# Kernel optimization log

Measured on AMD Instinct MI355X. Metric: run time of the kernel, lower is better.

The kernel has to match this reference:

```python
import jax, jax.numpy as jnp
import numpy as np


def setup_inputs() -> dict:
    B, I, H = 4096, 512, 1024
    key = jax.random.key(0)
    ks = jax.random.split(key, 10)
    return {
        "input": jax.random.normal(ks[0], (B, I), dtype=jnp.float32),
        "t": jax.random.uniform(ks[1], (B, 1), dtype=jnp.float32),
        "hx": jax.random.normal(ks[2], (B, H), dtype=jnp.float32),
        "cx": jax.random.normal(ks[3], (B, H), dtype=jnp.float32),
        "weight_ih": jax.random.normal(ks[4], (4 * H, I), dtype=jnp.float32),
        "weight_hh": jax.random.normal(ks[5], (4 * H, H), dtype=jnp.float32),
        "bias_ih": jax.random.normal(ks[6], (4 * H,), dtype=jnp.float32),
        "bias_hh": jax.random.normal(ks[7], (4 * H,), dtype=jnp.float32),
        "W_decomp": jax.random.normal(ks[8], (H, H), dtype=jnp.float32),
        "b_decomp": jax.random.normal(ks[9], (H,), dtype=jnp.float32),
    }


def reference(input, t, hx, cx, weight_ih, weight_hh, bias_ih, bias_hh, W_decomp, b_decomp):
    H = W_decomp.shape[0]
    # gates: [B, 4H]
    gates = input @ weight_ih.T + bias_ih + hx @ weight_hh.T + bias_hh
    ingate, forgetgate, cellgate, outgate = jnp.split(gates, 4, axis=1)
    # time-decay factor g(t): elementwise 1/t where t != 0, broadcast [B,1] -> [B,H]
    T = jnp.where(t != 0, 1.0 / jnp.where(t != 0, t, 1.0), 0.0)  # [B, 1]
    T = jnp.broadcast_to(T, (t.shape[0], H))
    # T-LSTM cell-state decomposition
    C_ST = jnp.tanh(cx @ W_decomp + b_decomp)
    cx_adj = cx - C_ST + T * C_ST
    ingate = jax.nn.sigmoid(ingate)
    forgetgate = jax.nn.sigmoid(forgetgate)
    cellgate = jnp.tanh(cellgate)
    outgate = jax.nn.sigmoid(outgate)
    cy = forgetgate * cx_adj + ingate * cellgate
    hy = outgate * jnp.tanh(cy)
    return (hy, cy)
```

## Files before the change

### kernel.cpp

```cpp
#include <hip/hip_runtime.h>
#include <cstdint>


typedef __attribute__((ext_vector_type(8))) __bf16 bf16x8;
typedef __attribute__((ext_vector_type(4))) float f32x4;

__device__ __forceinline__ unsigned short f2bf_rn(float f) {
  unsigned int u = __float_as_uint(f);
  unsigned int r = u + 0x7fffu + ((u >> 16) & 1u);
  return (unsigned short)(r >> 16);
}
__device__ __forceinline__ float bf2f(unsigned short h) {
  return __uint_as_float(((unsigned int)h) << 16);
}
__device__ __forceinline__ float sigm_f(float x) {
  return 1.0f / (1.0f + __expf(-x));
}
__device__ __forceinline__ float tanh_f(float x) {
  return 1.0f - 2.0f / (__expf(2.0f * x) + 1.0f);
}
__device__ __forceinline__ void gl_lds16(const void* g, void* l) {
  __builtin_amdgcn_global_load_lds(
      (const __attribute__((address_space(1))) void*)g,
      (__attribute__((address_space(3))) void*)l, 16, 0, 0);
}

__global__ __launch_bounds__(384) void prep_k(
    const float* __restrict__ input, const float* __restrict__ hx,
    const float* __restrict__ w_ih, const float* __restrict__ w_hh,
    const float* __restrict__ cx,
    unsigned short* __restrict__ Xhi, unsigned short* __restrict__ Xlo,
    unsigned short* __restrict__ Whi, unsigned short* __restrict__ Wlo,
    unsigned short* __restrict__ Chi, unsigned short* __restrict__ Clo) {
  const int bid = blockIdx.x;
  const int k = threadIdx.x << 2;
  const float* src;
  unsigned short *hi, *lo;
  if (bid < 4096) {
    const long m = bid;
    src = (k < 512) ? (input + m * 512 + k) : (hx + m * 1024 + (k - 512));
    hi = Xhi + m * 1536 + k;
    lo = Xlo + m * 1536 + k;
  } else if (bid < 8192) {
    const int n = bid - 4096;
    const int g = n >> 10;
    const int h = n & 1023;
    const long nd = ((long)(h >> 4) << 6) | (g << 4) | (h & 15);
    src = (k < 512) ? (w_ih + (long)n * 512 + k) : (w_hh + (long)n * 1024 + (k - 512));
    hi = Whi + nd * 1536 + k;
    lo = Wlo + nd * 1536 + k;
  } else {
    if (k >= 1024) return;
    const long m = bid - 8192;
    src = cx + m * 1024 + k;
    hi = Chi + m * 1024 + k;
    lo = Clo + m * 1024 + k;
  }
  float4 v = *(const float4*)src;
  ushort4 hv, lv;
  hv.x = f2bf_rn(v.x); lv.x = f2bf_rn(v.x - bf2f(hv.x));
  hv.y = f2bf_rn(v.y); lv.y = f2bf_rn(v.y - bf2f(hv.y));
  hv.z = f2bf_rn(v.z); lv.z = f2bf_rn(v.z - bf2f(hv.z));
  hv.w = f2bf_rn(v.w); lv.w = f2bf_rn(v.w - bf2f(hv.w));
  *(ushort4*)hi = hv;
  *(ushort4*)lo = lv;
}

__global__ void transpose_split_k(const float* __restrict__ W, int Ndim,
                                  unsigned short* __restrict__ Thi,
                                  unsigned short* __restrict__ Tlo) {
  __shared__ float tile[64][65];
  const int bx = blockIdx.x * 64;
  const int by = blockIdx.y * 64;
  const int tx = threadIdx.x;
  for (int r = threadIdx.y; r < 64; r += 4)
    tile[r][tx] = W[(long)(by + r) * Ndim + bx + tx];
  __syncthreads();
  for (int r = threadIdx.y; r < 64; r += 4) {
    float v = tile[tx][r];
    unsigned short h = f2bf_rn(v);
    long o = (long)(bx + r) * Ndim + by + tx;
    Thi[o] = h;
    Tlo[o] = f2bf_rn(v - bf2f(h));
  }
}

__global__ __launch_bounds__(512, 2) void gemm_mega(
    const unsigned short* __restrict__ Xh, const unsigned short* __restrict__ Xl,
    const unsigned short* __restrict__ Wh, const unsigned short* __restrict__ Wl,
    const unsigned short* __restrict__ Ch, const unsigned short* __restrict__ Cl,
    const unsigned short* __restrict__ Dh, const unsigned short* __restrict__ Dl,
    const float* __restrict__ b_ih, const float* __restrict__ b_hh,
    const float* __restrict__ b_d, const float* __restrict__ cx,
    const float* __restrict__ t, float* __restrict__ out) {
  __shared__ __align__(16) unsigned short sAh[2][8192];
  __shared__ __align__(16) unsigned short sAl[2][8192];
  __shared__ __align__(16) unsigned short sBh[2][4096];
  __shared__ __align__(16) unsigned short sBl[2][4096];

  const int swz = ((blockIdx.x & 7) << 6) | (blockIdx.x >> 3);
  const int n_blk = swz & 31;
  const int m_blk = swz >> 5;
  const int m0 = m_blk * 256;
  const int n0 = n_blk * 128;
  const int h0 = n_blk * 32;

  const int tid = threadIdx.x;
  const int wave = tid >> 6;
  const int lane = tid & 63;
  const int wr = wave >> 1;
  const int wc = wave & 1;
  const int srow = lane >> 2;
  const int ssw = (((lane & 3) ^ ((lane >> 3) & 3)) << 3);
  const int fm = lane & 15;
  const int fq = lane >> 4;
  const int psw = (fq ^ ((fm >> 1) & 3)) << 3;

#define STAGE1(B_, KT_)                                                        \
  {                                                                            \
    const long gA0 = (long)(m0 + wave * 32 + srow) * 1024 + (KT_) + ssw;       \
    gl_lds16(Ch + gA0, &sAh[B_][(wave * 32) * 32]);                            \
    gl_lds16(Cl + gA0, &sAl[B_][(wave * 32) * 32]);                            \
    const long gA1 = gA0 + 16 * 1024;                                          \
    gl_lds16(Ch + gA1, &sAh[B_][(wave * 32 + 16) * 32]);                       \
    gl_lds16(Cl + gA1, &sAl[B_][(wave * 32 + 16) * 32]);                       \
    if (wave < 4) {                                                            \
      const int rb = (wave & 1) * 16;                                          \
      const long gD = (long)(h0 + rb + srow) * 1024 + (KT_) + ssw;             \
      if (wave & 2) gl_lds16(Dl + gD, &sBl[B_][rb * 32]);                      \
      else          gl_lds16(Dh + gD, &sBh[B_][rb * 32]);                      \
    }                                                                          \
  }

#define STAGE2(B_, KT_)                                                        \
  {                                                                            \
    const long gA0 = (long)(m0 + wave * 32 + srow) * 1536 + (KT_) + ssw;       \
    gl_lds16(Xh + gA0, &sAh[B_][(wave * 32) * 32]);                            \
    gl_lds16(Xl + gA0, &sAl[B_][(wave * 32) * 32]);                            \
    const long gA1 = gA0 + 16 * 1536;                                          \
    gl_lds16(Xh + gA1, &sAh[B_][(wave * 32 + 16) * 32]);                       \
    gl_lds16(Xl + gA1, &sAl[B_][(wave * 32 + 16) * 32]);                       \
    const long gB0 = (long)(n0 + wave * 16 + srow) * 1536 + (KT_) + ssw;       \
    gl_lds16(Wh + gB0, &sBh[B_][(wave * 16) * 32]);                            \
    gl_lds16(Wl + gB0, &sBl[B_][(wave * 16) * 32]);                            \
  }

  f32x4 dacc[4];
#pragma unroll
  for (int i = 0; i < 4; ++i) dacc[i] = {0.f, 0.f, 0.f, 0.f};

  STAGE1(0, 0);
#pragma unroll 2
  for (int it = 0; it < 32; ++it) {
    const int b = it & 1;
    if (it < 31) {
      STAGE1(b ^ 1, (it + 1) * 32);
      if (wave < 4) asm volatile("s_waitcnt vmcnt(5)" ::: "memory");
      else          asm volatile("s_waitcnt vmcnt(4)" ::: "memory");
    } else {
      asm volatile("s_waitcnt vmcnt(0)" ::: "memory");
    }
    __builtin_amdgcn_s_barrier();
    bf16x8 ah[4], al[4];
#pragma unroll
    for (int mf = 0; mf < 4; ++mf) {
      const int ao = (wr * 64 + mf * 16 + fm) * 32 + psw;
      ah[mf] = *(const bf16x8*)&sAh[b][ao];
      al[mf] = *(const bf16x8*)&sAl[b][ao];
    }
    const int bo = (wc * 16 + fm) * 32 + psw;
    const bf16x8 bh = *(const bf16x8*)&sBh[b][bo];
    const bf16x8 bl = *(const bf16x8*)&sBl[b][bo];
    __builtin_amdgcn_s_setprio(1);
#pragma unroll
    for (int mf = 0; mf < 4; ++mf) {
      dacc[mf] = __builtin_amdgcn_mfma_f32_16x16x32_bf16(ah[mf], bh, dacc[mf], 0, 0, 0);
      dacc[mf] = __builtin_amdgcn_mfma_f32_16x16x32_bf16(ah[mf], bl, dacc[mf], 0, 0, 0);
      dacc[mf] = __builtin_amdgcn_mfma_f32_16x16x32_bf16(al[mf], bh, dacc[mf], 0, 0, 0);
    }
    __builtin_amdgcn_s_setprio(0);
    __builtin_amdgcn_s_barrier();
  }

  f32x4 acc[4][4];
#pragma unroll
  for (int i = 0; i < 4; ++i)
#pragma unroll
    for (int j = 0; j < 4; ++j) acc[i][j] = {0.f, 0.f, 0.f, 0.f};

  STAGE2(0, 0);
#pragma unroll 2
  for (int it = 0; it < 48; ++it) {
    const int b = it & 1;
    if (it < 47) {
      STAGE2(b ^ 1, (it + 1) * 32);
      asm volatile("s_waitcnt vmcnt(6)" ::: "memory");
    } else {
      asm volatile("s_waitcnt vmcnt(0)" ::: "memory");
    }
    __builtin_amdgcn_s_barrier();
    bf16x8 ah[4], al[4], bh[4], bl[4];
#pragma unroll
    for (int mf = 0; mf < 4; ++mf) {
      const int ao = (wr * 64 + mf * 16 + fm) * 32 + psw;
      ah[mf] = *(const bf16x8*)&sAh[b][ao];
      al[mf] = *(const bf16x8*)&sAl[b][ao];
    }
#pragma unroll
    for (int nf = 0; nf < 4; ++nf) {
      const int bo = (wc * 64 + nf * 16 + fm) * 32 + psw;
      bh[nf] = *(const bf16x8*)&sBh[b][bo];
      bl[nf] = *(const bf16x8*)&sBl[b][bo];
    }
    __builtin_amdgcn_s_setprio(1);
#pragma unroll
    for (int nf = 0; nf < 4; ++nf)
#pragma unroll
      for (int mf = 0; mf < 4; ++mf) {
        acc[mf][nf] = __builtin_amdgcn_mfma_f32_16x16x32_bf16(ah[mf], bh[nf], acc[mf][nf], 0, 0, 0);
        acc[mf][nf] = __builtin_amdgcn_mfma_f32_16x16x32_bf16(ah[mf], bl[nf], acc[mf][nf], 0, 0, 0);
        acc[mf][nf] = __builtin_amdgcn_mfma_f32_16x16x32_bf16(al[mf], bh[nf], acc[mf][nf], 0, 0, 0);
      }
    __builtin_amdgcn_s_setprio(0);
    __builtin_amdgcn_s_barrier();
  }

  const int h = h0 + wc * 16 + fm;
  const float bi  = b_ih[h]        + b_hh[h];
  const float bff = b_ih[1024 + h] + b_hh[1024 + h];
  const float bg  = b_ih[2048 + h] + b_hh[2048 + h];
  const float bo2 = b_ih[3072 + h] + b_hh[3072 + h];
  const float bd  = b_d[h];
#pragma unroll
  for (int mf = 0; mf < 4; ++mf) {
#pragma unroll
    for (int r = 0; r < 4; ++r) {
      const int m = m0 + wr * 64 + mf * 16 + fq * 4 + r;
      const float tv = t[m];
      const float T = (tv != 0.0f) ? (1.0f / tv) : 0.0f;
      const float cst = tanh_f(dacc[mf][r] + bd);
      const float cadj = cx[(long)m * 1024 + h] + (T - 1.0f) * cst;
      const float ig = sigm_f(acc[mf][0][r] + bi);
      const float fg = sigm_f(acc[mf][1][r] + bff);
      const float cg = tanh_f(acc[mf][2][r] + bg);
      const float og = sigm_f(acc[mf][3][r] + bo2);
      const float cyv = fg * cadj + ig * cg;
      const float hyv = og * tanh_f(cyv);
      out[(long)m * 1024 + h] = hyv;
      out[4096L * 1024 + (long)m * 1024 + h] = cyv;
    }
  }
#undef STAGE1
#undef STAGE2
}

extern "C" void kernel_launch(void* const* d_in, const int* in_sizes, int n_in,
                              void* d_out, int out_size, void* d_ws, size_t ws_size,
                              hipStream_t stream) {
  const float* input = (const float*)d_in[0];
  const float* t     = (const float*)d_in[1];
  const float* hx    = (const float*)d_in[2];
  const float* cx    = (const float*)d_in[3];
  const float* w_ih  = (const float*)d_in[4];
  const float* w_hh  = (const float*)d_in[5];
  const float* b_ih  = (const float*)d_in[6];
  const float* b_hh  = (const float*)d_in[7];
  const float* Wd    = (const float*)d_in[8];
  const float* b_d   = (const float*)d_in[9];

  const long B = 4096, H = 1024, KX = 1536, NG = 4096;

  char* ws = (char*)d_ws;
  unsigned short* Xhi = (unsigned short*)ws; ws += B * KX * 2;
  unsigned short* Xlo = (unsigned short*)ws; ws += B * KX * 2;
  unsigned short* Whi = (unsigned short*)ws; ws += NG * KX * 2;
  unsigned short* Wlo = (unsigned short*)ws; ws += NG * KX * 2;
  unsigned short* Chi = (unsigned short*)ws; ws += B * H * 2;
  unsigned short* Clo = (unsigned short*)ws; ws += B * H * 2;
  unsigned short* Dhi = (unsigned short*)ws; ws += H * H * 2;
  unsigned short* Dlo = (unsigned short*)ws; ws += H * H * 2;

  prep_k<<<12288, 384, 0, stream>>>(input, hx, w_ih, w_hh, cx,
                                    Xhi, Xlo, Whi, Wlo, Chi, Clo);
  transpose_split_k<<<dim3(16, 16), dim3(64, 4), 0, stream>>>(Wd, 1024, Dhi, Dlo);
  gemm_mega<<<512, 512, 0, stream>>>(Xhi, Xlo, Whi, Wlo, Chi, Clo, Dhi, Dlo,
                                     b_ih, b_hh, b_d, cx, t, (float*)d_out);
}
```

Before: 360.0 us.

## Fold Wd transpose into prep kernel and shrink GEMM tile to single-buffered 128x128

```diff
diff --git a/kernel.cpp b/kernel.cpp
--- a/kernel.cpp
+++ b/kernel.cpp
@@ -28,11 +28,31 @@
 __global__ __launch_bounds__(384) void prep_k(
     const float* __restrict__ input, const float* __restrict__ hx,
     const float* __restrict__ w_ih, const float* __restrict__ w_hh,
-    const float* __restrict__ cx,
+    const float* __restrict__ cx, const float* __restrict__ Wd,
     unsigned short* __restrict__ Xhi, unsigned short* __restrict__ Xlo,
     unsigned short* __restrict__ Whi, unsigned short* __restrict__ Wlo,
-    unsigned short* __restrict__ Chi, unsigned short* __restrict__ Clo) {
+    unsigned short* __restrict__ Chi, unsigned short* __restrict__ Clo,
+    unsigned short* __restrict__ Dhi, unsigned short* __restrict__ Dlo) {
   const int bid = blockIdx.x;
+  if (bid >= 12288) {
+    __shared__ float tile[64][65];
+    const int tb = bid - 12288;
+    const int bx = (tb & 15) * 64;
+    const int by = (tb >> 4) * 64;
+    const int tx = threadIdx.x & 63;
+    const int ty = threadIdx.x >> 6;
+    for (int r = ty; r < 64; r += 6)
+      tile[r][tx] = Wd[(long)(by + r) * 1024 + bx + tx];
+    __syncthreads();
+    for (int r = ty; r < 64; r += 6) {
+      float v = tile[tx][r];
+      unsigned short h = f2bf_rn(v);
+      long o = (long)(bx + r) * 1024 + by + tx;
+      Dhi[o] = h;
+      Dlo[o] = f2bf_rn(v - bf2f(h));
+    }
+    return;
+  }
   const int k = threadIdx.x << 2;
   const float* src;
   unsigned short *hi, *lo;
@@ -66,26 +86,7 @@
   *(ushort4*)lo = lv;
 }
 
-__global__ void transpose_split_k(const float* __restrict__ W, int Ndim,
-                                  unsigned short* __restrict__ Thi,
-                                  unsigned short* __restrict__ Tlo) {
-  __shared__ float tile[64][65];
-  const int bx = blockIdx.x * 64;
-  const int by = blockIdx.y * 64;
-  const int tx = threadIdx.x;
-  for (int r = threadIdx.y; r < 64; r += 4)
-    tile[r][tx] = W[(long)(by + r) * Ndim + bx + tx];
-  __syncthreads();
-  for (int r = threadIdx.y; r < 64; r += 4) {
-    float v = tile[tx][r];
-    unsigned short h = f2bf_rn(v);
-    long o = (long)(bx + r) * Ndim + by + tx;
-    Thi[o] = h;
-    Tlo[o] = f2bf_rn(v - bf2f(h));
-  }
-}
-
-__global__ __launch_bounds__(512, 2) void gemm_mega(
+__global__ __launch_bounds__(256) void gemm_mega(
     const unsigned short* __restrict__ Xh, const unsigned short* __restrict__ Xl,
     const unsigned short* __restrict__ Wh, const unsigned short* __restrict__ Wl,
     const unsigned short* __restrict__ Ch, const unsigned short* __restrict__ Cl,
@@ -93,15 +94,15 @@
     const float* __restrict__ b_ih, const float* __restrict__ b_hh,
     const float* __restrict__ b_d, const float* __restrict__ cx,
     const float* __restrict__ t, float* __restrict__ out) {
-  __shared__ __align__(16) unsigned short sAh[2][8192];
-  __shared__ __align__(16) unsigned short sAl[2][8192];
-  __shared__ __align__(16) unsigned short sBh[2][4096];
-  __shared__ __align__(16) unsigned short sBl[2][4096];
-
-  const int swz = ((blockIdx.x & 7) << 6) | (blockIdx.x >> 3);
+  __shared__ __align__(16) unsigned short sAh[128 * 32];
+  __shared__ __align__(16) unsigned short sAl[128 * 32];
+  __shared__ __align__(16) unsigned short sBh[128 * 32];
+  __shared__ __align__(16) unsigned short sBl[128 * 32];
+
+  const int swz = ((blockIdx.x & 7) << 7) | (blockIdx.x >> 3);
   const int n_blk = swz & 31;
   const int m_blk = swz >> 5;
-  const int m0 = m_blk * 256;
+  const int m0 = m_blk * 128;
   const int n0 = n_blk * 128;
   const int h0 = n_blk * 32;
 
@@ -116,70 +117,42 @@
   const int fq = lane >> 4;
   const int psw = (fq ^ ((fm >> 1) & 3)) << 3;
 
-#define STAGE1(B_, KT_)                                                        \
-  {                                                                            \
-    const long gA0 = (long)(m0 + wave * 32 + srow) * 1024 + (KT_) + ssw;       \
-    gl_lds16(Ch + gA0, &sAh[B_][(wave * 32) * 32]);                            \
-    gl_lds16(Cl + gA0, &sAl[B_][(wave * 32) * 32]);                            \
-    const long gA1 = gA0 + 16 * 1024;                                          \
-    gl_lds16(Ch + gA1, &sAh[B_][(wave * 32 + 16) * 32]);                       \
-    gl_lds16(Cl + gA1, &sAl[B_][(wave * 32 + 16) * 32]);                       \
-    if (wave < 4) {                                                            \
-      const int rb = (wave & 1) * 16;                                          \
-      const long gD = (long)(h0 + rb + srow) * 1024 + (KT_) + ssw;             \
-      if (wave & 2) gl_lds16(Dl + gD, &sBl[B_][rb * 32]);                      \
-      else          gl_lds16(Dh + gD, &sBh[B_][rb * 32]);                      \
-    }                                                                          \
-  }
-
-#define STAGE2(B_, KT_)                                                        \
-  {                                                                            \
-    const long gA0 = (long)(m0 + wave * 32 + srow) * 1536 + (KT_) + ssw;       \
-    gl_lds16(Xh + gA0, &sAh[B_][(wave * 32) * 32]);                            \
-    gl_lds16(Xl + gA0, &sAl[B_][(wave * 32) * 32]);                            \
-    const long gA1 = gA0 + 16 * 1536;                                          \
-    gl_lds16(Xh + gA1, &sAh[B_][(wave * 32 + 16) * 32]);                       \
-    gl_lds16(Xl + gA1, &sAl[B_][(wave * 32 + 16) * 32]);                       \
-    const long gB0 = (long)(n0 + wave * 16 + srow) * 1536 + (KT_) + ssw;       \
-    gl_lds16(Wh + gB0, &sBh[B_][(wave * 16) * 32]);                            \
-    gl_lds16(Wl + gB0, &sBl[B_][(wave * 16) * 32]);                            \
-  }
-
   f32x4 dacc[4];
 #pragma unroll
   for (int i = 0; i < 4; ++i) dacc[i] = {0.f, 0.f, 0.f, 0.f};
 
-  STAGE1(0, 0);
-#pragma unroll 2
-  for (int it = 0; it < 32; ++it) {
-    const int b = it & 1;
-    if (it < 31) {
-      STAGE1(b ^ 1, (it + 1) * 32);
-      if (wave < 4) asm volatile("s_waitcnt vmcnt(5)" ::: "memory");
-      else          asm volatile("s_waitcnt vmcnt(4)" ::: "memory");
-    } else {
-      asm volatile("s_waitcnt vmcnt(0)" ::: "memory");
-    }
-    __builtin_amdgcn_s_barrier();
+  for (int kt = 0; kt < 1024; kt += 32) {
+#pragma unroll
+    for (int r = 0; r < 2; ++r) {
+      const int rowb = r * 64 + wave * 16;
+      const long gA = (long)(m0 + rowb + srow) * 1024 + kt + ssw;
+      gl_lds16(Ch + gA, sAh + rowb * 32);
+      gl_lds16(Cl + gA, sAl + rowb * 32);
+    }
+    {
+      const int rb = (wave & 1) * 16;
+      const long gD = (long)(h0 + rb + srow) * 1024 + kt + ssw;
+      if (wave & 2) gl_lds16(Dl + gD, sBl + rb * 32);
+      else          gl_lds16(Dh + gD, sBh + rb * 32);
+    }
+    __syncthreads();
     bf16x8 ah[4], al[4];
 #pragma unroll
     for (int mf = 0; mf < 4; ++mf) {
       const int ao = (wr * 64 + mf * 16 + fm) * 32 + psw;
-      ah[mf] = *(const bf16x8*)&sAh[b][ao];
-      al[mf] = *(const bf16x8*)&sAl[b][ao];
+      ah[mf] = *(const bf16x8*)(sAh + ao);
+      al[mf] = *(const bf16x8*)(sAl + ao);
     }
     const int bo = (wc * 16 + fm) * 32 + psw;
-    const bf16x8 bh = *(const bf16x8*)&sBh[b][bo];
-    const bf16x8 bl = *(const bf16x8*)&sBl[b][bo];
-    __builtin_amdgcn_s_setprio(1);
+    const bf16x8 bh = *(const bf16x8*)(sBh + bo);
+    const bf16x8 bl = *(const bf16x8*)(sBl + bo);
 #pragma unroll
     for (int mf = 0; mf < 4; ++mf) {
       dacc[mf] = __builtin_amdgcn_mfma_f32_16x16x32_bf16(ah[mf], bh, dacc[mf], 0, 0, 0);
       dacc[mf] = __builtin_amdgcn_mfma_f32_16x16x32_bf16(ah[mf], bl, dacc[mf], 0, 0, 0);
       dacc[mf] = __builtin_amdgcn_mfma_f32_16x16x32_bf16(al[mf], bh, dacc[mf], 0, 0, 0);
     }
-    __builtin_amdgcn_s_setprio(0);
-    __builtin_amdgcn_s_barrier();
+    __syncthreads();
   }
 
   f32x4 acc[4][4];
@@ -188,31 +161,31 @@
 #pragma unroll
     for (int j = 0; j < 4; ++j) acc[i][j] = {0.f, 0.f, 0.f, 0.f};
 
-  STAGE2(0, 0);
-#pragma unroll 2
-  for (int it = 0; it < 48; ++it) {
-    const int b = it & 1;
-    if (it < 47) {
-      STAGE2(b ^ 1, (it + 1) * 32);
-      asm volatile("s_waitcnt vmcnt(6)" ::: "memory");
-    } else {
-      asm volatile("s_waitcnt vmcnt(0)" ::: "memory");
-    }
-    __builtin_amdgcn_s_barrier();
+  for (int kt = 0; kt < 1536; kt += 32) {
+#pragma unroll
+    for (int r = 0; r < 2; ++r) {
+      const int rowb = r * 64 + wave * 16;
+      const long gA = (long)(m0 + rowb + srow) * 1536 + kt + ssw;
+      const long gB = (long)(n0 + rowb + srow) * 1536 + kt + ssw;
+      gl_lds16(Xh + gA, sAh + rowb * 32);
+      gl_lds16(Xl + gA, sAl + rowb * 32);
+      gl_lds16(Wh + gB, sBh + rowb * 32);
+      gl_lds16(Wl + gB, sBl + rowb * 32);
+    }
+    __syncthreads();
     bf16x8 ah[4], al[4], bh[4], bl[4];
 #pragma unroll
     for (int mf = 0; mf < 4; ++mf) {
       const int ao = (wr * 64 + mf * 16 + fm) * 32 + psw;
-      ah[mf] = *(const bf16x8*)&sAh[b][ao];
-      al[mf] = *(const bf16x8*)&sAl[b][ao];
+      ah[mf] = *(const bf16x8*)(sAh + ao);
+      al[mf] = *(const bf16x8*)(sAl + ao);
     }
 #pragma unroll
     for (int nf = 0; nf < 4; ++nf) {
       const int bo = (wc * 64 + nf * 16 + fm) * 32 + psw;
-      bh[nf] = *(const bf16x8*)&sBh[b][bo];
-      bl[nf] = *(const bf16x8*)&sBl[b][bo];
-    }
-    __builtin_amdgcn_s_setprio(1);
+      bh[nf] = *(const bf16x8*)(sBh + bo);
+      bl[nf] = *(const bf16x8*)(sBl + bo);
+    }
 #pragma unroll
     for (int nf = 0; nf < 4; ++nf)
 #pragma unroll
@@ -221,8 +194,7 @@
         acc[mf][nf] = __builtin_amdgcn_mfma_f32_16x16x32_bf16(ah[mf], bl[nf], acc[mf][nf], 0, 0, 0);
         acc[mf][nf] = __builtin_amdgcn_mfma_f32_16x16x32_bf16(al[mf], bh[nf], acc[mf][nf], 0, 0, 0);
       }
-    __builtin_amdgcn_s_setprio(0);
-    __builtin_amdgcn_s_barrier();
+    __syncthreads();
   }
 
   const int h = h0 + wc * 16 + fm;
@@ -250,8 +222,6 @@
       out[4096L * 1024 + (long)m * 1024 + h] = cyv;
     }
   }
-#undef STAGE1
-#undef STAGE2
 }
 
 extern "C" void kernel_launch(void* const* d_in, const int* in_sizes, int n_in,
@@ -280,9 +250,8 @@
   unsigned short* Dhi = (unsigned short*)ws; ws += H * H * 2;
   unsigned short* Dlo = (unsigned short*)ws; ws += H * H * 2;
 
-  prep_k<<<12288, 384, 0, stream>>>(input, hx, w_ih, w_hh, cx,
-                                    Xhi, Xlo, Whi, Wlo, Chi, Clo);
-  transpose_split_k<<<dim3(16, 16), dim3(64, 4), 0, stream>>>(Wd, 1024, Dhi, Dlo);
-  gemm_mega<<<512, 512, 0, stream>>>(Xhi, Xlo, Whi, Wlo, Chi, Clo, Dhi, Dlo,
-                                     b_ih, b_hh, b_d, cx, t, (float*)d_out);
-}
+  prep_k<<<12544, 384, 0, stream>>>(input, hx, w_ih, w_hh, cx, Wd,
+                                    Xhi, Xlo, Whi, Wlo, Chi, Clo, Dhi, Dlo);
+  gemm_mega<<<1024, 256, 0, stream>>>(Xhi, Xlo, Whi, Wlo, Chi, Clo, Dhi, Dlo,
+                                      b_ih, b_hh, b_d, cx, t, (float*)d_out);
+}
```

Measured after the change: 339.6 us. -5.7%, faster.
